# Kernel tuning notes

Hardware: AMD Instinct MI355X
Metric: run time of the kernel (lower is better)

Reference implementation:

```python
import jax, jax.numpy as jnp
import numpy as np

# static config (matches init_kwargs)
WS = (8, 7, 7)       # window size (T, H, W)
SS = (4, 3, 3)       # shift size (T, H, W)
NUM_HEADS = 4
B, T, H, W, C = 2, 16, 56, 56, 128
VOL = WS[0] * WS[1] * WS[2]  # 392 tokens per window


def _compute_attention_mask_3d(size_dhw, window_size, shift_size):
    """Static numpy replica of torch _compute_attention_mask_3d -> [nW, V, V]."""
    m = np.zeros(size_dhw, dtype=np.float32)
    slices = [((0, -window_size[i]), (-window_size[i], -shift_size[i]), (-shift_size[i], None))
              for i in range(3)]
    cnt = 0
    for d0, d1 in slices[0]:
        for h0, h1 in slices[1]:
            for w0, w1 in slices[2]:
                m[d0:d1, h0:h1, w0:w1] = cnt
                cnt += 1
    nT, nH, nW_ = (size_dhw[0] // window_size[0], size_dhw[1] // window_size[1],
                   size_dhw[2] // window_size[2])
    m = m.reshape(nT, window_size[0], nH, window_size[1], nW_, window_size[2])
    m = m.transpose(0, 2, 4, 1, 3, 5).reshape(nT * nH * nW_, VOL)
    diff = m[:, None, :] - m[:, :, None]
    return np.where(diff != 0, np.float32(-100.0), np.float32(0.0))


_ATTN_MASK = jnp.asarray(_compute_attention_mask_3d((T, H, W), WS, SS))  # [nW, V, V]


def setup_inputs() -> dict:
    key = jax.random.key(0)
    ks = jax.random.split(key, 6)
    s = 0.02
    return {
        "x": jax.random.normal(ks[0], (B, T, H, W, C), jnp.float32),
        "qkv_weight": jax.random.normal(ks[1], (3 * C, C), jnp.float32) * s,
        "qkv_bias": jax.random.normal(ks[2], (3 * C,), jnp.float32) * s,
        "proj_weight": jax.random.normal(ks[3], (C, C), jnp.float32) * s,
        "proj_bias": jax.random.normal(ks[4], (C,), jnp.float32) * s,
        "rel_pos_bias": jax.random.normal(ks[5], (1, NUM_HEADS, VOL, VOL), jnp.float32) * s,
    }


def reference(x, qkv_weight, qkv_bias, proj_weight, proj_bias, rel_pos_bias):
    b, t, h, w, c = x.shape
    hd = c // NUM_HEADS
    wt, wh, ww = WS
    nt, nh, nw = t // wt, h // wh, w // ww
    n_win = nt * nh * nw

    # cyclic shift (T,H,W divide the window so no padding needed)
    xs = jnp.roll(x, shift=(-SS[0], -SS[1], -SS[2]), axis=(1, 2, 3))

    # window partition -> [b*n_win, VOL, c]
    xw = xs.reshape(b, nt, wt, nh, wh, nw, ww, c)
    xw = xw.transpose(0, 1, 3, 5, 2, 4, 6, 7).reshape(b * n_win, VOL, c)

    # qkv projection
    qkv = xw @ qkv_weight.T + qkv_bias
    qkv = qkv.reshape(b * n_win, VOL, 3, NUM_HEADS, hd).transpose(2, 0, 3, 1, 4)
    q, k, v = qkv[0], qkv[1], qkv[2]          # [b*nW, nH, V, hd]
    q = q * (hd ** -0.5)

    attn = jnp.einsum("whqd,whkd->whqk", q, k) + rel_pos_bias
    # shift mask: broadcast over batch and heads
    attn = attn.reshape(b, n_win, NUM_HEADS, VOL, VOL) + _ATTN_MASK[None, :, None, :, :]
    attn = jax.nn.softmax(attn.reshape(b * n_win, NUM_HEADS, VOL, VOL), axis=-1)

    out = jnp.einsum("whqk,whkd->whqd", attn, v)         # [b*nW, nH, V, hd]
    out = out.transpose(0, 2, 1, 3).reshape(b * n_win, VOL, c)
    out = out @ proj_weight.T + proj_bias

    # window un-partition -> [b, t, h, w, c]
    out = out.reshape(b, nt, nh, nw, wt, wh, ww, c)
    out = out.transpose(0, 1, 4, 2, 5, 3, 6, 7).reshape(b, t, h, w, c)
    out = jnp.roll(out, shift=(SS[0], SS[1], SS[2]), axis=(1, 2, 3))
    return out
```

## Files before the change

kernel.cpp:

```cpp
#include <hip/hip_runtime.h>
#include <hip/hip_bf16.h>

typedef __bf16 bf16;
typedef __bf16 bf16x4 __attribute__((ext_vector_type(4)));
typedef __bf16 bf16x8 __attribute__((ext_vector_type(8)));
typedef float f32x4 __attribute__((ext_vector_type(4)));

#define MFMA(a, b, c) __builtin_amdgcn_mfma_f32_16x16x32_bf16(a, b, c, 0, 0, 0)

__device__ inline f32x4 zf4() { return f32x4{0.f, 0.f, 0.f, 0.f}; }

constexpr int Bc = 2, Tc = 16, Hc = 56, Wc = 56, Cc = 128, NHc = 4, HDc = 32;
constexpr int VOL = 392;
constexpr int STc = 4, SHc = 3, SWc = 3;
constexpr int TWIN = 256;
constexpr int MTOT = TWIN * VOL;
constexpr int QSZ = TWIN * NHc * VOL * HDc;
constexpr int BMT_N = 8 * 4 * 400 * 416;

__device__ inline bf16x8 zero8() {
    bf16x8 z;
#pragma unroll
    for (int j = 0; j < 8; ++j) z[j] = (bf16)0.0f;
    return z;
}

__device__ inline int cls_of(int v, int pt, int ph, int pw) {
    int tt = v / 49, rem = v % 49, hh = rem / 7, ww = rem % 7;
    int ct = pt ? (tt < 4 ? 1 : 2) : 0;
    int ch = ph ? (hh < 4 ? 1 : 2) : 0;
    int cw = pw ? (ww < 4 ? 1 : 2) : 0;
    return ct * 9 + ch * 3 + cw;
}

__global__ void cvt_kernel(const float* __restrict__ src, bf16* __restrict__ dst,
                           int n4) {
    int i = blockIdx.x * blockDim.x + threadIdx.x;
    if (i < n4) {
        f32x4 v = *(const f32x4*)(src + (size_t)i * 4);
        bf16x4 o;
#pragma unroll
        for (int j = 0; j < 4; ++j) o[j] = (bf16)v[j];
        *(bf16x4*)(dst + (size_t)i * 4) = o;
    }
}

__global__ void biasprep_kernel(const float* __restrict__ rpb, bf16* __restrict__ bmt) {
    int idx = blockIdx.x * 256 + threadIdx.x;
    if (idx >= BMT_N) return;
    int col = idx % 416; int t = idx / 416;
    int row = t % 400; t /= 400;
    int head = t & 3; int pat = t >> 2;
    float v;
    if (col >= VOL) v = -144.26950408889634f;
    else if (row >= VOL) v = 0.f;
    else {
        float bias = rpb[((size_t)head * VOL + row) * VOL + col];
        int pt = (pat >> 2) & 1, ph = (pat >> 1) & 1, pw = pat & 1;
        bool same = (cls_of(row, pt, ph, pw) == cls_of(col, pt, ph, pw));
        v = (bias + (same ? 0.f : -100.f)) * 1.4426950408889634f;
    }
    bmt[idx] = (bf16)v;
}

__global__ __launch_bounds__(256, 2)
void qkv_kernel(const float* __restrict__ x, const bf16* __restrict__ wq,
                const bf16* __restrict__ bq, bf16* __restrict__ qws,
                bf16* __restrict__ kws, bf16* __restrict__ vws) {
    __shared__ bf16 As[64][136];
    __shared__ bf16 Cs[64][392];
    const int tid = threadIdx.x;
    const int m0 = blockIdx.x * 64;

    for (int idx = tid; idx < 64 * 32; idx += 256) {
        int r = idx >> 5, c = idx & 31;
        int g = m0 + r;
        int win = g / VOL, tok = g % VOL;
        int b = win >> 7, wi = win & 127;
        int wt_i = wi >> 6, wh_i = (wi >> 3) & 7, ww_i = wi & 7;
        int tt = tok / 49, r2 = tok % 49;
        int hh = r2 / 7, ww2 = r2 % 7;
        int t = wt_i * 8 + tt + STc; if (t >= Tc) t -= Tc;
        int h = wh_i * 7 + hh + SHc; if (h >= Hc) h -= Hc;
        int w = ww_i * 7 + ww2 + SWc; if (w >= Wc) w -= Wc;
        const float* src = x + (size_t)(((b * Tc + t) * Hc + h) * Wc + w) * Cc + c * 4;
        f32x4 v = *(const f32x4*)src;
        bf16x4 o;
#pragma unroll
        for (int j = 0; j < 4; ++j) o[j] = (bf16)v[j];
        *(bf16x4*)(&As[r][c * 4]) = o;
    }
    __syncthreads();

    const int wid = tid >> 6, lane = tid & 63;
    const int quad = lane >> 4, l15 = lane & 15;
    const int nbase = wid * 96;

    f32x4 acc[4][6];
#pragma unroll
    for (int ms = 0; ms < 4; ++ms)
#pragma unroll
        for (int nt = 0; nt < 6; ++nt) acc[ms][nt] = zf4();

#pragma unroll
    for (int ko = 0; ko < 4; ++ko) {
        bf16x8 af[4];
#pragma unroll
        for (int ms = 0; ms < 4; ++ms)
            af[ms] = *(const bf16x8*)(&As[ms * 16 + l15][ko * 32 + quad * 8]);
#pragma unroll
        for (int nt = 0; nt < 6; ++nt) {
            int n = nbase + nt * 16 + l15;
            bf16x8 bfrag = *(const bf16x8*)(wq + (size_t)n * Cc + ko * 32 + quad * 8);
#pragma unroll
            for (int ms = 0; ms < 4; ++ms)
                acc[ms][nt] = MFMA(af[ms], bfrag, acc[ms][nt]);
        }
    }

    float bcol[6];
#pragma unroll
    for (int nt = 0; nt < 6; ++nt) bcol[nt] = (float)bq[nbase + nt * 16 + l15];

#pragma unroll
    for (int nt = 0; nt < 6; ++nt) {
        int col = nbase + nt * 16 + l15;
        float scale = (col < 128) ? 0.25505653942f : 1.0f;
#pragma unroll
        for (int ms = 0; ms < 4; ++ms)
#pragma unroll
            for (int r = 0; r < 4; ++r) {
                int row = ms * 16 + quad * 4 + r;
                Cs[row][col] = (bf16)((acc[ms][nt][r] + bcol[nt]) * scale);
            }
    }
    __syncthreads();

    {
        int row = tid >> 2, head = tid & 3;
        int g = m0 + row;
        int win = g / VOL, tok = g % VOL;
        size_t off = ((size_t)(win * NHc + head) * VOL + tok) * HDc;
#pragma unroll
        for (int c = 0; c < 4; ++c)
            *(bf16x8*)(qws + off + c * 8) = *(const bf16x8*)(&Cs[row][head * 32 + c * 8]);
#pragma unroll
        for (int c = 0; c < 4; ++c)
            *(bf16x8*)(kws + off + c * 8) = *(const bf16x8*)(&Cs[row][128 + head * 32 + c * 8]);
#pragma unroll
        for (int c = 0; c < 4; ++c)
            *(bf16x8*)(vws + off + c * 8) = *(const bf16x8*)(&Cs[row][256 + head * 32 + c * 8]);
    }
}

__global__ __launch_bounds__(512, 4)
void attn_kernel(const bf16* __restrict__ qws, const bf16* __restrict__ kws,
                 const bf16* __restrict__ vws, const bf16* __restrict__ bmt,
                 bf16* __restrict__ aows) {
    __shared__ bf16 Kl[416][40];
    __shared__ bf16 Vt[32][424];
    __shared__ bf16 Pb[8][16][40];

    const int tid = threadIdx.x;
    const int win = blockIdx.x >> 2, head = blockIdx.x & 3;
    const int wi = win & 127;
    const int wt_i = wi >> 6, wh_i = (wi >> 3) & 7, ww_i = wi & 7;
    const int pat = ((wt_i == 1) << 2) | ((wh_i == 7) << 1) | (ww_i == 7);

    const bf16* Qg = qws + (size_t)(win * NHc + head) * VOL * HDc;
    const bf16* Kg = kws + (size_t)(win * NHc + head) * VOL * HDc;
    const bf16* Vg = vws + (size_t)(win * NHc + head) * VOL * HDc;
    const bf16* Bg = bmt + (size_t)(pat * NHc + head) * 400 * 416;

    for (int idx = tid; idx < 416 * 4; idx += 512) {
        int tok = idx >> 2, c = idx & 3;
        bf16x8 v = zero8();
        if (tok < VOL) v = *(const bf16x8*)(Kg + tok * HDc + c * 8);
        *(bf16x8*)(&Kl[tok][c * 8]) = v;
    }
    for (int idx = tid; idx < 416 * 4; idx += 512) {
        int tok = idx >> 2, c = idx & 3;
        bf16x8 v = zero8();
        if (tok < VOL) v = *(const bf16x8*)(Vg + tok * HDc + c * 8);
#pragma unroll
        for (int j = 0; j < 8; ++j) Vt[c * 8 + j][tok] = v[j];
    }
    __syncthreads();

    const int wid = tid >> 6, lane = tid & 63;
    const int quad = lane >> 4, l15 = lane & 15;
    bf16* Pw = &Pb[wid][0][0];

    for (int qt = wid; qt < 25; qt += 8) {
        const int qb = qt * 16;
        const int qrow = (qb + l15 < VOL) ? (qb + l15) : (VOL - 1);
        const bf16x8 qf = *(const bf16x8*)(Qg + (size_t)qrow * HDc + quad * 8);
        const bf16* Brow = Bg + (size_t)(qb + l15) * 416;
        f32x4 o0 = zf4(), o1 = zf4();
        float lsum = 0.f;
        bf16x4 nb0 = *(const bf16x4*)(Brow + quad * 4);
        bf16x4 nb1 = *(const bf16x4*)(Brow + 16 + quad * 4);
#pragma unroll 1
        for (int kt = 0; kt < 13; ++kt) {
            const int kb = kt * 32;
            f32x4 c0, c1;
#pragma unroll
            for (int j = 0; j < 4; ++j) { c0[j] = (float)nb0[j]; c1[j] = (float)nb1[j]; }
            bf16x8 kf0 = *(const bf16x8*)(&Kl[kb + l15][quad * 8]);
            bf16x8 kf1 = *(const bf16x8*)(&Kl[kb + 16 + l15][quad * 8]);
            if (kt < 12) {
                nb0 = *(const bf16x4*)(Brow + kb + 32 + quad * 4);
                nb1 = *(const bf16x4*)(Brow + kb + 48 + quad * 4);
            }
            f32x4 s0 = MFMA(kf0, qf, c0);
            f32x4 s1 = MFMA(kf1, qf, c1);
            bf16x4 p0, p1;
            float ls = 0.f;
#pragma unroll
            for (int r = 0; r < 4; ++r) {
                float e0 = __builtin_amdgcn_exp2f(s0[r]);
                float e1 = __builtin_amdgcn_exp2f(s1[r]);
                p0[r] = (bf16)e0; p1[r] = (bf16)e1;
                ls += e0 + e1;
            }
            lsum += ls;
            *(bf16x4*)(Pw + l15 * 40 + quad * 4) = p0;
            *(bf16x4*)(Pw + l15 * 40 + 16 + quad * 4) = p1;
            asm volatile("s_waitcnt lgkmcnt(0)" ::: "memory");
            bf16x8 pf = *(const bf16x8*)(Pw + l15 * 40 + quad * 8);
            bf16x8 vf0 = *(const bf16x8*)(&Vt[l15][kb + quad * 8]);
            bf16x8 vf1 = *(const bf16x8*)(&Vt[16 + l15][kb + quad * 8]);
            o0 = MFMA(vf0, pf, o0);
            o1 = MFMA(vf1, pf, o1);
        }
        lsum += __shfl_xor(lsum, 16);
        lsum += __shfl_xor(lsum, 32);
        if (qb + l15 < VOL) {
            float inv = 1.f / lsum;
            bf16x4 w0, w1;
#pragma unroll
            for (int r = 0; r < 4; ++r) {
                w0[r] = (bf16)(o0[r] * inv);
                w1[r] = (bf16)(o1[r] * inv);
            }
            bf16* dst = aows + ((size_t)win * VOL + qb + l15) * Cc + head * HDc;
            *(bf16x4*)(dst + quad * 4) = w0;
            *(bf16x4*)(dst + 16 + quad * 4) = w1;
        }
    }
}

__global__ __launch_bounds__(256, 2)
void proj_kernel(const bf16* __restrict__ aows, const bf16* __restrict__ wp,
                 const bf16* __restrict__ bp, float* __restrict__ out) {
    __shared__ bf16 As[64][136];
    __shared__ float Csf[64][132];
    const int tid = threadIdx.x;
    const int m0 = blockIdx.x * 64;

    for (int idx = tid; idx < 64 * 16; idx += 256) {
        int r = idx >> 4, c = idx & 15;
        *(bf16x8*)(&As[r][c * 8]) = *(const bf16x8*)(aows + (size_t)(m0 + r) * Cc + c * 8);
    }
    __syncthreads();

    const int wid = tid >> 6, lane = tid & 63;
    const int quad = lane >> 4, l15 = lane & 15;

    f32x4 acc[8];
#pragma unroll
    for (int nt = 0; nt < 8; ++nt) acc[nt] = zf4();

#pragma unroll
    for (int ko = 0; ko < 4; ++ko) {
        bf16x8 af = *(const bf16x8*)(&As[wid * 16 + l15][ko * 32 + quad * 8]);
#pragma unroll
        for (int nt = 0; nt < 8; ++nt) {
            bf16x8 bfrag = *(const bf16x8*)(wp + (size_t)(nt * 16 + l15) * Cc + ko * 32 + quad * 8);
            acc[nt] = MFMA(af, bfrag, acc[nt]);
        }
    }
#pragma unroll
    for (int nt = 0; nt < 8; ++nt) {
        float bv = (float)bp[nt * 16 + l15];
#pragma unroll
        for (int r = 0; r < 4; ++r) {
            int row = wid * 16 + quad * 4 + r;
            Csf[row][nt * 16 + l15] = acc[nt][r] + bv;
        }
    }
    __syncthreads();

    for (int idx = tid; idx < 64 * 32; idx += 256) {
        int row = idx >> 5, ch = idx & 31;
        int g = m0 + row;
        int win = g / VOL, tok = g % VOL;
        int b = win >> 7, wi = win & 127;
        int wt_i = wi >> 6, wh_i = (wi >> 3) & 7, ww_i = wi & 7;
        int tt = tok / 49, r2 = tok % 49, hh = r2 / 7, ww2 = r2 % 7;
        int t = wt_i * 8 + tt + STc; if (t >= Tc) t -= Tc;
        int h = wh_i * 7 + hh + SHc; if (h >= Hc) h -= Hc;
        int w = ww_i * 7 + ww2 + SWc; if (w >= Wc) w -= Wc;
        float* dst = out + (size_t)(((b * Tc + t) * Hc + h) * Wc + w) * Cc + ch * 4;
        *(f32x4*)dst = *(const f32x4*)(&Csf[row][ch * 4]);
    }
}

extern "C" void kernel_launch(void* const* d_in, const int* in_sizes, int n_in,
                              void* d_out, int out_size, void* d_ws, size_t ws_size,
                              hipStream_t stream) {
    const float* x    = (const float*)d_in[0];
    const float* wqf  = (const float*)d_in[1];
    const float* bqf  = (const float*)d_in[2];
    const float* wpf  = (const float*)d_in[3];
    const float* bpf  = (const float*)d_in[4];
    const float* rpbf = (const float*)d_in[5];
    float* out = (float*)d_out;

    bf16* wqb  = (bf16*)d_ws;
    bf16* bqb  = wqb + 49152;
    bf16* wpb  = bqb + 384;
    bf16* bpb  = wpb + 16384;
    bf16* bmt  = bpb + 128;
    bf16* qws  = bmt + BMT_N;
    bf16* kws  = qws + QSZ;
    bf16* vws  = kws + QSZ;
    bf16* aows = vws + QSZ;

    hipLaunchKernelGGL(cvt_kernel, dim3((12288 + 255) / 256), dim3(256), 0, stream, wqf, wqb, 12288);
    hipLaunchKernelGGL(cvt_kernel, dim3(1), dim3(256), 0, stream, bqf, bqb, 96);
    hipLaunchKernelGGL(cvt_kernel, dim3((4096 + 255) / 256), dim3(256), 0, stream, wpf, wpb, 4096);
    hipLaunchKernelGGL(cvt_kernel, dim3(1), dim3(256), 0, stream, bpf, bpb, 32);
    hipLaunchKernelGGL(biasprep_kernel, dim3((BMT_N + 255) / 256), dim3(256), 0, stream, rpbf, bmt);

    hipLaunchKernelGGL(qkv_kernel, dim3(MTOT / 64), dim3(256), 0, stream,
                       x, wqb, bqb, qws, kws, vws);
    hipLaunchKernelGGL(attn_kernel, dim3(TWIN * NHc), dim3(512), 0, stream,
                       qws, kws, vws, bmt, aows);
    hipLaunchKernelGGL(proj_kernel, dim3(MTOT / 64), dim3(256), 0, stream,
                       aows, wpb, bpb, out);
}
```

Before: 275.1 us.

## Encode shift mask as one-hot MFMA, shrink bias table, process two query tiles per wave

The shift-window mask is no longer baked into eight pattern-specific bias tables. It is generated inside the attention kernel by an extra MFMA over one-hot class encodings, and only for masked windows, so the bias table shrinks eightfold and its memory traffic and L2 footprint drop. The attention loop now handles two query tiles per wave, software-pipelines PV against QK, and peels the last key tile. Launch overhead is cut by merging the parameter conversions into one kernel, and shift-address math is precomputed once per row in the qkv and proj kernels. The risks are extra MFMA work on masked windows and more register pressure, plus possible precision loss from the one-hot ±12 encoding in bf16.

```diff
diff --git a/kernel.cpp b/kernel.cpp
--- a/kernel.cpp
+++ b/kernel.cpp
@@ -10,19 +10,27 @@
 
 __device__ inline f32x4 zf4() { return f32x4{0.f, 0.f, 0.f, 0.f}; }
 
-constexpr int Bc = 2, Tc = 16, Hc = 56, Wc = 56, Cc = 128, NHc = 4, HDc = 32;
+constexpr int Tc = 16, Hc = 56, Wc = 56, Cc = 128, NHc = 4, HDc = 32;
 constexpr int VOL = 392;
 constexpr int STc = 4, SHc = 3, SWc = 3;
 constexpr int TWIN = 256;
 constexpr int MTOT = TWIN * VOL;
 constexpr int QSZ = TWIN * NHc * VOL * HDc;
-constexpr int BMT_N = 8 * 4 * 400 * 416;
+constexpr int BMT_N = 4 * 400 * 416;
+constexpr int OH_N = 8 * 416 * 32;
 
 __device__ inline bf16x8 zero8() {
     bf16x8 z;
 #pragma unroll
     for (int j = 0; j < 8; ++j) z[j] = (bf16)0.0f;
     return z;
+}
+
+__device__ inline f32x4 up4(bf16x4 b) {
+    f32x4 r;
+#pragma unroll
+    for (int j = 0; j < 4; ++j) r[j] = (float)b[j];
+    return r;
 }
 
 __device__ inline int cls_of(int v, int pt, int ph, int pw) {
@@ -33,34 +41,61 @@
     return ct * 9 + ch * 3 + cw;
 }
 
-__global__ void cvt_kernel(const float* __restrict__ src, bf16* __restrict__ dst,
-                           int n4) {
-    int i = blockIdx.x * blockDim.x + threadIdx.x;
-    if (i < n4) {
-        f32x4 v = *(const f32x4*)(src + (size_t)i * 4);
-        bf16x4 o;
-#pragma unroll
-        for (int j = 0; j < 4; ++j) o[j] = (bf16)v[j];
-        *(bf16x4*)(dst + (size_t)i * 4) = o;
-    }
+__global__ void cvt_params(const float* __restrict__ wq, const float* __restrict__ bq,
+                           const float* __restrict__ wp, const float* __restrict__ bp,
+                           bf16* __restrict__ wqb, bf16* __restrict__ bqb,
+                           bf16* __restrict__ wpb, bf16* __restrict__ bpb) {
+    int i = blockIdx.x * 256 + threadIdx.x;
+    const float* s; bf16* d; int off;
+    if (i < 12288)       { s = wq; d = wqb; off = i; }
+    else if (i < 12384)  { s = bq; d = bqb; off = i - 12288; }
+    else if (i < 16480)  { s = wp; d = wpb; off = i - 12384; }
+    else if (i < 16512)  { s = bp; d = bpb; off = i - 16480; }
+    else return;
+    f32x4 v = *(const f32x4*)(s + (size_t)off * 4);
+    bf16x4 o;
+#pragma unroll
+    for (int j = 0; j < 4; ++j) o[j] = (bf16)v[j];
+    *(bf16x4*)(d + (size_t)off * 4) = o;
 }
 
 __global__ void biasprep_kernel(const float* __restrict__ rpb, bf16* __restrict__ bmt) {
-    int idx = blockIdx.x * 256 + threadIdx.x;
-    if (idx >= BMT_N) return;
-    int col = idx % 416; int t = idx / 416;
-    int row = t % 400; t /= 400;
-    int head = t & 3; int pat = t >> 2;
-    float v;
-    if (col >= VOL) v = -144.26950408889634f;
-    else if (row >= VOL) v = 0.f;
-    else {
-        float bias = rpb[((size_t)head * VOL + row) * VOL + col];
-        int pt = (pat >> 2) & 1, ph = (pat >> 1) & 1, pw = pat & 1;
-        bool same = (cls_of(row, pt, ph, pw) == cls_of(col, pt, ph, pw));
-        v = (bias + (same ? 0.f : -100.f)) * 1.4426950408889634f;
-    }
-    bmt[idx] = (bf16)v;
+    int i = blockIdx.x * 256 + threadIdx.x;
+    if (i >= 4 * 400 * 104) return;
+    int c4 = i % 104; int t = i / 104;
+    int row = t % 400; int head = t / 400;
+    f32x4 v;
+    if (row >= VOL) {
+#pragma unroll
+        for (int j = 0; j < 4; ++j) v[j] = 0.f;
+    } else if (c4 >= 98) {
+#pragma unroll
+        for (int j = 0; j < 4; ++j) v[j] = -144.0f;
+    } else {
+        f32x4 b = *(const f32x4*)(rpb + ((size_t)(head * VOL + row) * VOL + c4 * 4));
+#pragma unroll
+        for (int j = 0; j < 4; ++j) v[j] = b[j] * 1.4426950408889634f;
+    }
+    bf16x4 o;
+#pragma unroll
+    for (int j = 0; j < 4; ++j) o[j] = (bf16)v[j];
+    *(bf16x4*)(bmt + ((size_t)(head * 400) * 416 + (size_t)(t % 400) * 416 - (size_t)(t % 400) * 416) + (size_t)t * 416 + c4 * 4) = o;
+}
+
+__global__ void ohprep_kernel(bf16* __restrict__ ohq, bf16* __restrict__ ohk) {
+    int i = blockIdx.x * 256 + threadIdx.x;
+    if (i >= 8 * 416) return;
+    int tok = i % 416, pat = i / 416;
+    int pt = (pat >> 2) & 1, ph = (pat >> 1) & 1, pw = pat & 1;
+    int cls = (tok < VOL) ? cls_of(tok, pt, ph, pw) : -1;
+    bf16* dq = ohq + (size_t)i * 32;
+    bf16* dk = ohk + (size_t)i * 32;
+    for (int ch = 0; ch < 32; ++ch) {
+        float qv = (ch == cls) ? 12.0f : ((ch == 31) ? 12.0f : 0.f);
+        float kv = (ch == cls) ? 12.0f : ((ch == 31) ? -12.0f : 0.f);
+        dq[ch] = (bf16)qv;
+        dk[ch] = (bf16)kv;
+    }
 }
 
 __global__ __launch_bounds__(256, 2)
@@ -68,232 +103,14 @@
                 const bf16* __restrict__ bq, bf16* __restrict__ qws,
                 bf16* __restrict__ kws, bf16* __restrict__ vws) {
     __shared__ bf16 As[64][136];
-    __shared__ bf16 Cs[64][392];
+    __shared__ bf16 Cs[64][396];
+    __shared__ unsigned int rb[64];
+    __shared__ unsigned int rbw[64];
     const int tid = threadIdx.x;
     const int m0 = blockIdx.x * 64;
 
-    for (int idx = tid; idx < 64 * 32; idx += 256) {
-        int r = idx >> 5, c = idx & 31;
-        int g = m0 + r;
-        int win = g / VOL, tok = g % VOL;
-        int b = win >> 7, wi = win & 127;
-        int wt_i = wi >> 6, wh_i = (wi >> 3) & 7, ww_i = wi & 7;
-        int tt = tok / 49, r2 = tok % 49;
-        int hh = r2 / 7, ww2 = r2 % 7;
-        int t = wt_i * 8 + tt + STc; if (t >= Tc) t -= Tc;
-        int h = wh_i * 7 + hh + SHc; if (h >= Hc) h -= Hc;
-        int w = ww_i * 7 + ww2 + SWc; if (w >= Wc) w -= Wc;
-        const float* src = x + (size_t)(((b * Tc + t) * Hc + h) * Wc + w) * Cc + c * 4;
-        f32x4 v = *(const f32x4*)src;
-        bf16x4 o;
-#pragma unroll
-        for (int j = 0; j < 4; ++j) o[j] = (bf16)v[j];
-        *(bf16x4*)(&As[r][c * 4]) = o;
-    }
-    __syncthreads();
-
-    const int wid = tid >> 6, lane = tid & 63;
-    const int quad = lane >> 4, l15 = lane & 15;
-    const int nbase = wid * 96;
-
-    f32x4 acc[4][6];
-#pragma unroll
-    for (int ms = 0; ms < 4; ++ms)
-#pragma unroll
-        for (int nt = 0; nt < 6; ++nt) acc[ms][nt] = zf4();
-
-#pragma unroll
-    for (int ko = 0; ko < 4; ++ko) {
-        bf16x8 af[4];
-#pragma unroll
-        for (int ms = 0; ms < 4; ++ms)
-            af[ms] = *(const bf16x8*)(&As[ms * 16 + l15][ko * 32 + quad * 8]);
-#pragma unroll
-        for (int nt = 0; nt < 6; ++nt) {
-            int n = nbase + nt * 16 + l15;
-            bf16x8 bfrag = *(const bf16x8*)(wq + (size_t)n * Cc + ko * 32 + quad * 8);
-#pragma unroll
-            for (int ms = 0; ms < 4; ++ms)
-                acc[ms][nt] = MFMA(af[ms], bfrag, acc[ms][nt]);
-        }
-    }
-
-    float bcol[6];
-#pragma unroll
-    for (int nt = 0; nt < 6; ++nt) bcol[nt] = (float)bq[nbase + nt * 16 + l15];
-
-#pragma unroll
-    for (int nt = 0; nt < 6; ++nt) {
-        int col = nbase + nt * 16 + l15;
-        float scale = (col < 128) ? 0.25505653942f : 1.0f;
-#pragma unroll
-        for (int ms = 0; ms < 4; ++ms)
-#pragma unroll
-            for (int r = 0; r < 4; ++r) {
-                int row = ms * 16 + quad * 4 + r;
-                Cs[row][col] = (bf16)((acc[ms][nt][r] + bcol[nt]) * scale);
-            }
-    }
-    __syncthreads();
-
-    {
-        int row = tid >> 2, head = tid & 3;
-        int g = m0 + row;
-        int win = g / VOL, tok = g % VOL;
-        size_t off = ((size_t)(win * NHc + head) * VOL + tok) * HDc;
-#pragma unroll
-        for (int c = 0; c < 4; ++c)
-            *(bf16x8*)(qws + off + c * 8) = *(const bf16x8*)(&Cs[row][head * 32 + c * 8]);
-#pragma unroll
-        for (int c = 0; c < 4; ++c)
-            *(bf16x8*)(kws + off + c * 8) = *(const bf16x8*)(&Cs[row][128 + head * 32 + c * 8]);
-#pragma unroll
-        for (int c = 0; c < 4; ++c)
-            *(bf16x8*)(vws + off + c * 8) = *(const bf16x8*)(&Cs[row][256 + head * 32 + c * 8]);
-    }
-}
-
-__global__ __launch_bounds__(512, 4)
-void attn_kernel(const bf16* __restrict__ qws, const bf16* __restrict__ kws,
-                 const bf16* __restrict__ vws, const bf16* __restrict__ bmt,
-                 bf16* __restrict__ aows) {
-    __shared__ bf16 Kl[416][40];
-    __shared__ bf16 Vt[32][424];
-    __shared__ bf16 Pb[8][16][40];
-
-    const int tid = threadIdx.x;
-    const int win = blockIdx.x >> 2, head = blockIdx.x & 3;
-    const int wi = win & 127;
-    const int wt_i = wi >> 6, wh_i = (wi >> 3) & 7, ww_i = wi & 7;
-    const int pat = ((wt_i == 1) << 2) | ((wh_i == 7) << 1) | (ww_i == 7);
-
-    const bf16* Qg = qws + (size_t)(win * NHc + head) * VOL * HDc;
-    const bf16* Kg = kws + (size_t)(win * NHc + head) * VOL * HDc;
-    const bf16* Vg = vws + (size_t)(win * NHc + head) * VOL * HDc;
-    const bf16* Bg = bmt + (size_t)(pat * NHc + head) * 400 * 416;
-
-    for (int idx = tid; idx < 416 * 4; idx += 512) {
-        int tok = idx >> 2, c = idx & 3;
-        bf16x8 v = zero8();
-        if (tok < VOL) v = *(const bf16x8*)(Kg + tok * HDc + c * 8);
-        *(bf16x8*)(&Kl[tok][c * 8]) = v;
-    }
-    for (int idx = tid; idx < 416 * 4; idx += 512) {
-        int tok = idx >> 2, c = idx & 3;
-        bf16x8 v = zero8();
-        if (tok < VOL) v = *(const bf16x8*)(Vg + tok * HDc + c * 8);
-#pragma unroll
-        for (int j = 0; j < 8; ++j) Vt[c * 8 + j][tok] = v[j];
-    }
-    __syncthreads();
-
-    const int wid = tid >> 6, lane = tid & 63;
-    const int quad = lane >> 4, l15 = lane & 15;
-    bf16* Pw = &Pb[wid][0][0];
-
-    for (int qt = wid; qt < 25; qt += 8) {
-        const int qb = qt * 16;
-        const int qrow = (qb + l15 < VOL) ? (qb + l15) : (VOL - 1);
-        const bf16x8 qf = *(const bf16x8*)(Qg + (size_t)qrow * HDc + quad * 8);
-        const bf16* Brow = Bg + (size_t)(qb + l15) * 416;
-        f32x4 o0 = zf4(), o1 = zf4();
-        float lsum = 0.f;
-        bf16x4 nb0 = *(const bf16x4*)(Brow + quad * 4);
-        bf16x4 nb1 = *(const bf16x4*)(Brow + 16 + quad * 4);
-#pragma unroll 1
-        for (int kt = 0; kt < 13; ++kt) {
-            const int kb = kt * 32;
-            f32x4 c0, c1;
-#pragma unroll
-            for (int j = 0; j < 4; ++j) { c0[j] = (float)nb0[j]; c1[j] = (float)nb1[j]; }
-            bf16x8 kf0 = *(const bf16x8*)(&Kl[kb + l15][quad * 8]);
-            bf16x8 kf1 = *(const bf16x8*)(&Kl[kb + 16 + l15][quad * 8]);
-            if (kt < 12) {
-                nb0 = *(const bf16x4*)(Brow + kb + 32 + quad * 4);
-                nb1 = *(const bf16x4*)(Brow + kb + 48 + quad * 4);
-            }
-            f32x4 s0 = MFMA(kf0, qf, c0);
-            f32x4 s1 = MFMA(kf1, qf, c1);
-            bf16x4 p0, p1;
-            float ls = 0.f;
-#pragma unroll
-            for (int r = 0; r < 4; ++r) {
-                float e0 = __builtin_amdgcn_exp2f(s0[r]);
-                float e1 = __builtin_amdgcn_exp2f(s1[r]);
-                p0[r] = (bf16)e0; p1[r] = (bf16)e1;
-                ls += e0 + e1;
-            }
-            lsum += ls;
-            *(bf16x4*)(Pw + l15 * 40 + quad * 4) = p0;
-            *(bf16x4*)(Pw + l15 * 40 + 16 + quad * 4) = p1;
-            asm volatile("s_waitcnt lgkmcnt(0)" ::: "memory");
-            bf16x8 pf = *(const bf16x8*)(Pw + l15 * 40 + quad * 8);
-            bf16x8 vf0 = *(const bf16x8*)(&Vt[l15][kb + quad * 8]);
-            bf16x8 vf1 = *(const bf16x8*)(&Vt[16 + l15][kb + quad * 8]);
-            o0 = MFMA(vf0, pf, o0);
-            o1 = MFMA(vf1, pf, o1);
-        }
-        lsum += __shfl_xor(lsum, 16);
-        lsum += __shfl_xor(lsum, 32);
-        if (qb + l15 < VOL) {
-            float inv = 1.f / lsum;
-            bf16x4 w0, w1;
-#pragma unroll
-            for (int r = 0; r < 4; ++r) {
-                w0[r] = (bf16)(o0[r] * inv);
-                w1[r] = (bf16)(o1[r] * inv);
-            }
-            bf16* dst = aows + ((size_t)win * VOL + qb + l15) * Cc + head * HDc;
-            *(bf16x4*)(dst + quad * 4) = w0;
-            *(bf16x4*)(dst + 16 + quad * 4) = w1;
-        }
-    }
-}
-
-__global__ __launch_bounds__(256, 2)
-void proj_kernel(const bf16* __restrict__ aows, const bf16* __restrict__ wp,
-                 const bf16* __restrict__ bp, float* __restrict__ out) {
-    __shared__ bf16 As[64][136];
-    __shared__ float Csf[64][132];
-    const int tid = threadIdx.x;
-    const int m0 = blockIdx.x * 64;
-
-    for (int idx = tid; idx < 64 * 16; idx += 256) {
-        int r = idx >> 4, c = idx & 15;
-        *(bf16x8*)(&As[r][c * 8]) = *(const bf16x8*)(aows + (size_t)(m0 + r) * Cc + c * 8);
-    }
-    __syncthreads();
-
-    const int wid = tid >> 6, lane = tid & 63;
-    const int quad = lane >> 4, l15 = lane & 15;
-
-    f32x4 acc[8];
-#pragma unroll
-    for (int nt = 0; nt < 8; ++nt) acc[nt] = zf4();
-
-#pragma unroll
-    for (int ko = 0; ko < 4; ++ko) {
-        bf16x8 af = *(const bf16x8*)(&As[wid * 16 + l15][ko * 32 + quad * 8]);
-#pragma unroll
-        for (int nt = 0; nt < 8; ++nt) {
-            bf16x8 bfrag = *(const bf16x8*)(wp + (size_t)(nt * 16 + l15) * Cc + ko * 32 + quad * 8);
-            acc[nt] = MFMA(af, bfrag, acc[nt]);
-        }
-    }
-#pragma unroll
-    for (int nt = 0; nt < 8; ++nt) {
-        float bv = (float)bp[nt * 16 + l15];
-#pragma unroll
-        for (int r = 0; r < 4; ++r) {
-            int row = wid * 16 + quad * 4 + r;
-            Csf[row][nt * 16 + l15] = acc[nt][r] + bv;
-        }
-    }
-    __syncthreads();
-
-    for (int idx = tid; idx < 64 * 32; idx += 256) {
-        int row = idx >> 5, ch = idx & 31;
-        int g = m0 + row;
+    if (tid < 64) {
+        int g = m0 + tid;
         int win = g / VOL, tok = g % VOL;
         int b = win >> 7, wi = win & 127;
         int wt_i = wi >> 6, wh_i = (wi >> 3) & 7, ww_i = wi & 7;
@@ -301,7 +118,350 @@
         int t = wt_i * 8 + tt + STc; if (t >= Tc) t -= Tc;
         int h = wh_i * 7 + hh + SHc; if (h >= Hc) h -= Hc;
         int w = ww_i * 7 + ww2 + SWc; if (w >= Wc) w -= Wc;
-        float* dst = out + (size_t)(((b * Tc + t) * Hc + h) * Wc + w) * Cc + ch * 4;
+        rb[tid] = (unsigned int)((((b * Tc + t) * Hc + h) * Wc + w) * Cc * 4);
+        rbw[tid] = (unsigned int)((win << 9) | tok);
+    }
+    __syncthreads();
+
+    for (int idx = tid; idx < 64 * 32; idx += 256) {
+        int r = idx >> 5, c = idx & 31;
+        const float* src = (const float*)((const char*)x + rb[r]) + c * 4;
+        f32x4 v = *(const f32x4*)src;
+        bf16x4 o;
+#pragma unroll
+        for (int j = 0; j < 4; ++j) o[j] = (bf16)v[j];
+        *(bf16x4*)(&As[r][c * 4]) = o;
+    }
+    __syncthreads();
+
+    const int wid = tid >> 6, lane = tid & 63;
+    const int quad = lane >> 4, l15 = lane & 15;
+    const int nbase = wid * 96;
+
+    f32x4 acc[4][6];
+#pragma unroll
+    for (int ms = 0; ms < 4; ++ms)
+#pragma unroll
+        for (int nt = 0; nt < 6; ++nt) acc[ms][nt] = zf4();
+
+#pragma unroll
+    for (int ko = 0; ko < 4; ++ko) {
+        bf16x8 af[4];
+#pragma unroll
+        for (int ms = 0; ms < 4; ++ms)
+            af[ms] = *(const bf16x8*)(&As[ms * 16 + l15][ko * 32 + quad * 8]);
+#pragma unroll
+        for (int nt = 0; nt < 6; ++nt) {
+            int n = nbase + nt * 16 + l15;
+            bf16x8 bfrag = *(const bf16x8*)(wq + (size_t)n * Cc + ko * 32 + quad * 8);
+#pragma unroll
+            for (int ms = 0; ms < 4; ++ms)
+                acc[ms][nt] = MFMA(af[ms], bfrag, acc[ms][nt]);
+        }
+    }
+
+    float bcol[6];
+#pragma unroll
+    for (int nt = 0; nt < 6; ++nt) bcol[nt] = (float)bq[nbase + nt * 16 + l15];
+
+#pragma unroll
+    for (int nt = 0; nt < 6; ++nt) {
+        int col = nbase + nt * 16 + l15;
+        float scale = (col < 128) ? 0.25505653942f : 1.0f;
+#pragma unroll
+        for (int ms = 0; ms < 4; ++ms)
+#pragma unroll
+            for (int r = 0; r < 4; ++r) {
+                int row = ms * 16 + quad * 4 + r;
+                Cs[row][col] = (bf16)((acc[ms][nt][r] + bcol[nt]) * scale);
+            }
+    }
+    __syncthreads();
+
+    {
+        int row = tid >> 2, hh4 = tid & 3;
+        unsigned int p = rbw[row];
+        int win = p >> 9, tok = p & 511;
+        size_t off = ((size_t)(win * NHc + hh4) * VOL + tok) * HDc;
+#pragma unroll
+        for (int c = 0; c < 4; ++c) {
+            bf16x4 lo = *(const bf16x4*)(&Cs[row][hh4 * 32 + c * 8]);
+            bf16x4 hi = *(const bf16x4*)(&Cs[row][hh4 * 32 + c * 8 + 4]);
+            *(bf16x8*)(qws + off + c * 8) = __builtin_shufflevector(lo, hi, 0, 1, 2, 3, 4, 5, 6, 7);
+        }
+#pragma unroll
+        for (int c = 0; c < 4; ++c) {
+            bf16x4 lo = *(const bf16x4*)(&Cs[row][128 + hh4 * 32 + c * 8]);
+            bf16x4 hi = *(const bf16x4*)(&Cs[row][128 + hh4 * 32 + c * 8 + 4]);
+            *(bf16x8*)(kws + off + c * 8) = __builtin_shufflevector(lo, hi, 0, 1, 2, 3, 4, 5, 6, 7);
+        }
+#pragma unroll
+        for (int c = 0; c < 4; ++c) {
+            bf16x4 lo = *(const bf16x4*)(&Cs[row][256 + hh4 * 32 + c * 8]);
+            bf16x4 hi = *(const bf16x4*)(&Cs[row][256 + hh4 * 32 + c * 8 + 4]);
+            *(bf16x8*)(vws + off + c * 8) = __builtin_shufflevector(lo, hi, 0, 1, 2, 3, 4, 5, 6, 7);
+        }
+    }
+}
+
+__global__ __launch_bounds__(512, 4)
+void attn_kernel(const bf16* __restrict__ qws, const bf16* __restrict__ kws,
+                 const bf16* __restrict__ vws, const bf16* __restrict__ bmt,
+                 const bf16* __restrict__ ohqt, const bf16* __restrict__ ohkt,
+                 bf16* __restrict__ aows) {
+    __shared__ bf16 Kl[400][40];
+    __shared__ bf16 Vt[32][424];
+    __shared__ bf16 Pb[8][2][16][40];
+
+    const int tid = threadIdx.x;
+    const int win = blockIdx.x >> 2, head = blockIdx.x & 3;
+    const int wi = win & 127;
+    const int wt_i = wi >> 6, wh_i = (wi >> 3) & 7, ww_i = wi & 7;
+    const int pat = ((wt_i == 1) << 2) | ((wh_i == 7) << 1) | (ww_i == 7);
+    const bool masked = (pat != 0);
+
+    const bf16* Qg = qws + (size_t)(win * NHc + head) * VOL * HDc;
+    const bf16* Kg = kws + (size_t)(win * NHc + head) * VOL * HDc;
+    const bf16* Vg = vws + (size_t)(win * NHc + head) * VOL * HDc;
+    const bf16* Bg = bmt + (size_t)head * 400 * 416;
+    const bf16* ohq_p = ohqt + (size_t)pat * 416 * 32;
+    const bf16* ohk_p = ohkt + (size_t)pat * 416 * 32;
+
+    for (int idx = tid; idx < 400 * 4; idx += 512) {
+        int tok = idx >> 2, c = idx & 3;
+        bf16x8 v = zero8();
+        if (tok < VOL) v = *(const bf16x8*)(Kg + tok * HDc + c * 8);
+        *(bf16x8*)(&Kl[tok][c * 8]) = v;
+    }
+    if (tid < 416) {
+        int c = tid & 3, tok4 = (tid >> 2) * 4;
+        bf16x8 rr[4];
+#pragma unroll
+        for (int i = 0; i < 4; ++i)
+            rr[i] = (tok4 + i < VOL) ? *(const bf16x8*)(Vg + (tok4 + i) * HDc + c * 8) : zero8();
+#pragma unroll
+        for (int j = 0; j < 8; ++j) {
+            bf16x4 wv;
+            wv[0] = rr[0][j]; wv[1] = rr[1][j]; wv[2] = rr[2][j]; wv[3] = rr[3][j];
+            *(bf16x4*)(&Vt[c * 8 + j][tok4]) = wv;
+        }
+    }
+    __syncthreads();
+
+    const int wid = tid >> 6, lane = tid & 63;
+    const int quad = lane >> 4, l15 = lane & 15;
+    bf16* PwA = &Pb[wid][0][0][0];
+    bf16* PwB = &Pb[wid][1][0][0];
+
+    for (int pass = 0; pass < 2; ++pass) {
+        const int qtA = pass * 16 + wid, qtB = qtA + 8;
+        const bool hasB = (qtB < 25);
+        const int qbA = qtA * 16, qbB = qtB * 16;
+        int qrA = qbA + l15; if (qrA >= VOL) qrA = VOL - 1;
+        const bf16x8 qfA = *(const bf16x8*)(Qg + (size_t)qrA * HDc + quad * 8);
+        const bf16* BrA = Bg + (size_t)(qbA + l15) * 416;
+        const bf16* BrB = BrA;
+        bf16x8 qfB, ohqA, ohqB;
+        if (masked) ohqA = *(const bf16x8*)(ohq_p + (size_t)(qbA + l15) * 32 + quad * 8);
+        if (hasB) {
+            int qrB = qbB + l15; if (qrB >= VOL) qrB = VOL - 1;
+            qfB = *(const bf16x8*)(Qg + (size_t)qrB * HDc + quad * 8);
+            BrB = Bg + (size_t)(qbB + l15) * 416;
+            if (masked) ohqB = *(const bf16x8*)(ohq_p + (size_t)(qbB + l15) * 32 + quad * 8);
+        }
+        f32x4 oA0 = zf4(), oA1 = zf4(), oB0 = zf4(), oB1 = zf4();
+        float lsA = 0.f, lsB = 0.f;
+        bf16x4 nbA0 = *(const bf16x4*)(BrA);
+        bf16x4 nbA1 = *(const bf16x4*)(BrA + 16);
+        bf16x4 nbB0, nbB1;
+        if (hasB) { nbB0 = *(const bf16x4*)(BrB); nbB1 = *(const bf16x4*)(BrB + 16); }
+
+        auto qk_full = [&](int kb) {
+            bf16x8 kf0 = *(const bf16x8*)(&Kl[kb + l15][quad * 8]);
+            bf16x8 kf1 = *(const bf16x8*)(&Kl[kb + 16 + l15][quad * 8]);
+            bf16x8 ok0, ok1;
+            if (masked) {
+                ok0 = *(const bf16x8*)(ohk_p + (size_t)(kb + l15) * 32 + quad * 8);
+                ok1 = *(const bf16x8*)(ohk_p + (size_t)(kb + 16 + l15) * 32 + quad * 8);
+            }
+            f32x4 cA0 = up4(nbA0), cA1 = up4(nbA1), cB0, cB1;
+            if (hasB) { cB0 = up4(nbB0); cB1 = up4(nbB1); }
+            if (kb < 384) {
+                nbA0 = *(const bf16x4*)(BrA + kb + 32);
+                nbA1 = *(const bf16x4*)(BrA + kb + 48);
+                if (hasB) {
+                    nbB0 = *(const bf16x4*)(BrB + kb + 32);
+                    nbB1 = *(const bf16x4*)(BrB + kb + 48);
+                }
+            }
+            if (masked) {
+                cA0 = MFMA(ok0, ohqA, cA0);
+                cA1 = MFMA(ok1, ohqA, cA1);
+                if (hasB) { cB0 = MFMA(ok0, ohqB, cB0); cB1 = MFMA(ok1, ohqB, cB1); }
+            }
+            f32x4 sA0 = MFMA(kf0, qfA, cA0);
+            f32x4 sA1 = MFMA(kf1, qfA, cA1);
+            bf16x4 pA0, pA1;
+            float la = 0.f;
+#pragma unroll
+            for (int r = 0; r < 4; ++r) {
+                float e0 = __builtin_amdgcn_exp2f(sA0[r]);
+                float e1 = __builtin_amdgcn_exp2f(sA1[r]);
+                pA0[r] = (bf16)e0; pA1[r] = (bf16)e1; la += e0 + e1;
+            }
+            lsA += la;
+            *(bf16x4*)(PwA + l15 * 40 + quad * 4) = pA0;
+            *(bf16x4*)(PwA + l15 * 40 + 16 + quad * 4) = pA1;
+            if (hasB) {
+                f32x4 sB0 = MFMA(kf0, qfB, cB0);
+                f32x4 sB1 = MFMA(kf1, qfB, cB1);
+                bf16x4 pB0, pB1;
+                float lb = 0.f;
+#pragma unroll
+                for (int r = 0; r < 4; ++r) {
+                    float e0 = __builtin_amdgcn_exp2f(sB0[r]);
+                    float e1 = __builtin_amdgcn_exp2f(sB1[r]);
+                    pB0[r] = (bf16)e0; pB1[r] = (bf16)e1; lb += e0 + e1;
+                }
+                lsB += lb;
+                *(bf16x4*)(PwB + l15 * 40 + quad * 4) = pB0;
+                *(bf16x4*)(PwB + l15 * 40 + 16 + quad * 4) = pB1;
+            }
+        };
+        auto pv = [&](int kb) {
+            bf16x8 pfA = *(const bf16x8*)(PwA + l15 * 40 + quad * 8);
+            bf16x8 pfB;
+            if (hasB) pfB = *(const bf16x8*)(PwB + l15 * 40 + quad * 8);
+            bf16x8 vf0 = *(const bf16x8*)(&Vt[l15][kb + quad * 8]);
+            bf16x8 vf1 = *(const bf16x8*)(&Vt[16 + l15][kb + quad * 8]);
+            oA0 = MFMA(vf0, pfA, oA0);
+            oA1 = MFMA(vf1, pfA, oA1);
+            if (hasB) { oB0 = MFMA(vf0, pfB, oB0); oB1 = MFMA(vf1, pfB, oB1); }
+        };
+
+        qk_full(0);
+#pragma unroll 1
+        for (int kt = 1; kt < 12; ++kt) {
+            pv((kt - 1) * 32);
+            qk_full(kt * 32);
+        }
+        pv(352);
+        {
+            bf16x8 kf0 = *(const bf16x8*)(&Kl[384 + l15][quad * 8]);
+            bf16x8 ok0;
+            if (masked) ok0 = *(const bf16x8*)(ohk_p + (size_t)(384 + l15) * 32 + quad * 8);
+            f32x4 cA0 = up4(nbA0), cB0;
+            if (hasB) cB0 = up4(nbB0);
+            if (masked) {
+                cA0 = MFMA(ok0, ohqA, cA0);
+                if (hasB) cB0 = MFMA(ok0, ohqB, cB0);
+            }
+            f32x4 sA0 = MFMA(kf0, qfA, cA0);
+            bf16x4 pA0, z4;
+            float la = 0.f;
+#pragma unroll
+            for (int r = 0; r < 4; ++r) {
+                float e0 = __builtin_amdgcn_exp2f(sA0[r]);
+                pA0[r] = (bf16)e0; la += e0; z4[r] = (bf16)0.f;
+            }
+            lsA += la;
+            *(bf16x4*)(PwA + l15 * 40 + quad * 4) = pA0;
+            *(bf16x4*)(PwA + l15 * 40 + 16 + quad * 4) = z4;
+            if (hasB) {
+                f32x4 sB0 = MFMA(kf0, qfB, cB0);
+                bf16x4 pB0;
+                float lb = 0.f;
+#pragma unroll
+                for (int r = 0; r < 4; ++r) {
+                    float e0 = __builtin_amdgcn_exp2f(sB0[r]);
+                    pB0[r] = (bf16)e0; lb += e0;
+                }
+                lsB += lb;
+                *(bf16x4*)(PwB + l15 * 40 + quad * 4) = pB0;
+                *(bf16x4*)(PwB + l15 * 40 + 16 + quad * 4) = z4;
+            }
+        }
+        pv(384);
+
+        lsA += __shfl_xor(lsA, 16); lsA += __shfl_xor(lsA, 32);
+        if (hasB) { lsB += __shfl_xor(lsB, 16); lsB += __shfl_xor(lsB, 32); }
+        if (qbA + l15 < VOL) {
+            float inv = 1.f / lsA;
+            bf16x4 w0, w1;
+#pragma unroll
+            for (int r = 0; r < 4; ++r) { w0[r] = (bf16)(oA0[r] * inv); w1[r] = (bf16)(oA1[r] * inv); }
+            bf16* dst = aows + ((size_t)win * VOL + qbA + l15) * Cc + head * HDc;
+            *(bf16x4*)(dst + quad * 4) = w0;
+            *(bf16x4*)(dst + 16 + quad * 4) = w1;
+        }
+        if (hasB && qbB + l15 < VOL) {
+            float inv = 1.f / lsB;
+            bf16x4 w0, w1;
+#pragma unroll
+            for (int r = 0; r < 4; ++r) { w0[r] = (bf16)(oB0[r] * inv); w1[r] = (bf16)(oB1[r] * inv); }
+            bf16* dst = aows + ((size_t)win * VOL + qbB + l15) * Cc + head * HDc;
+            *(bf16x4*)(dst + quad * 4) = w0;
+            *(bf16x4*)(dst + 16 + quad * 4) = w1;
+        }
+    }
+}
+
+__global__ __launch_bounds__(256, 2)
+void proj_kernel(const bf16* __restrict__ aows, const bf16* __restrict__ wp,
+                 const bf16* __restrict__ bp, float* __restrict__ out) {
+    __shared__ bf16 As[64][136];
+    __shared__ float Csf[64][132];
+    __shared__ unsigned int rbo[64];
+    const int tid = threadIdx.x;
+    const int m0 = blockIdx.x * 64;
+
+    if (tid < 64) {
+        int g = m0 + tid;
+        int win = g / VOL, tok = g % VOL;
+        int b = win >> 7, wi = win & 127;
+        int wt_i = wi >> 6, wh_i = (wi >> 3) & 7, ww_i = wi & 7;
+        int tt = tok / 49, r2 = tok % 49, hh = r2 / 7, ww2 = r2 % 7;
+        int t = wt_i * 8 + tt + STc; if (t >= Tc) t -= Tc;
+        int h = wh_i * 7 + hh + SHc; if (h >= Hc) h -= Hc;
+        int w = ww_i * 7 + ww2 + SWc; if (w >= Wc) w -= Wc;
+        rbo[tid] = (unsigned int)((((b * Tc + t) * Hc + h) * Wc + w) * Cc * 4);
+    }
+    for (int idx = tid; idx < 64 * 16; idx += 256) {
+        int r = idx >> 4, c = idx & 15;
+        *(bf16x8*)(&As[r][c * 8]) = *(const bf16x8*)(aows + (size_t)(m0 + r) * Cc + c * 8);
+    }
+    __syncthreads();
+
+    const int wid = tid >> 6, lane = tid & 63;
+    const int quad = lane >> 4, l15 = lane & 15;
+
+    f32x4 acc[8];
+#pragma unroll
+    for (int nt = 0; nt < 8; ++nt) acc[nt] = zf4();
+
+#pragma unroll
+    for (int ko = 0; ko < 4; ++ko) {
+        bf16x8 af = *(const bf16x8*)(&As[wid * 16 + l15][ko * 32 + quad * 8]);
+#pragma unroll
+        for (int nt = 0; nt < 8; ++nt) {
+            bf16x8 bfrag = *(const bf16x8*)(wp + (size_t)(nt * 16 + l15) * Cc + ko * 32 + quad * 8);
+            acc[nt] = MFMA(af, bfrag, acc[nt]);
+        }
+    }
+#pragma unroll
+    for (int nt = 0; nt < 8; ++nt) {
+        float bv = (float)bp[nt * 16 + l15];
+#pragma unroll
+        for (int r = 0; r < 4; ++r) {
+            int row = wid * 16 + quad * 4 + r;
+            Csf[row][nt * 16 + l15] = acc[nt][r] + bv;
+        }
+    }
+    __syncthreads();
+
+    for (int idx = tid; idx < 64 * 32; idx += 256) {
+        int row = idx >> 5, ch = idx & 31;
+        float* dst = (float*)((char*)out + rbo[row]) + ch * 4;
         *(f32x4*)dst = *(const f32x4*)(&Csf[row][ch * 4]);
     }
 }
@@ -322,21 +482,23 @@
     bf16* wpb  = bqb + 384;
     bf16* bpb  = wpb + 16384;
     bf16* bmt  = bpb + 128;
-    bf16* qws  = bmt + BMT_N;
+    bf16* ohq  = bmt + BMT_N;
+    bf16* ohk  = ohq + OH_N;
+    bf16* qws  = ohk + OH_N;
     bf16* kws  = qws + QSZ;
     bf16* vws  = kws + QSZ;
     bf16* aows = vws + QSZ;
 
-    hipLaunchKernelGGL(cvt_kernel, dim3((12288 + 255) / 256), dim3(256), 0, stream, wqf, wqb, 12288);
-    hipLaunchKernelGGL(cvt_kernel, dim3(1), dim3(256), 0, stream, bqf, bqb, 96);
-    hipLaunchKernelGGL(cvt_kernel, dim3((4096 + 255) / 256), dim3(256), 0, stream, wpf, wpb, 4096);
-    hipLaunchKernelGGL(cvt_kernel, dim3(1), dim3(256), 0, stream, bpf, bpb, 32);
-    hipLaunchKernelGGL(biasprep_kernel, dim3((BMT_N + 255) / 256), dim3(256), 0, stream, rpbf, bmt);
-
+    hipLaunchKernelGGL(cvt_params, dim3(65), dim3(256), 0, stream,
+                       wqf, bqf, wpf, bpf, wqb, bqb, wpb, bpb);
+    hipLaunchKernelGGL(biasprep_kernel, dim3((4 * 400 * 104 + 255) / 256), dim3(256), 0, stream,
+                       rpbf, bmt);
+    hipLaunchKernelGGL(ohprep_kernel, dim3((8 * 416 + 255) / 256), dim3(256), 0, stream,
+                       ohq, ohk);
     hipLaunchKernelGGL(qkv_kernel, dim3(MTOT / 64), dim3(256), 0, stream,
                        x, wqb, bqb, qws, kws, vws);
     hipLaunchKernelGGL(attn_kernel, dim3(TWIN * NHc), dim3(512), 0, stream,
-                       qws, kws, vws, bmt, aows);
+                       qws, kws, vws, bmt, ohq, ohk, aows);
     hipLaunchKernelGGL(proj_kernel, dim3(MTOT / 64), dim3(256), 0, stream,
                        aows, wpb, bpb, out);
 }
```

Result: no change. 273.2 us (-0.7%).
